# Optimization experiments

Hardware: AMD Instinct MI355X
Metric: run time of the kernel (lower is better)

## Reference

```python
import jax, jax.numpy as jnp
import numpy as np

N_NODES = 50000
N_EDGES = 400000
NUM_FEATURES = 32
NUM_GRAPHS = 64
NUM_CLASSES = 2


def setup_inputs() -> dict:
    key = jax.random.key(0)
    ks = jax.random.split(key, 24)
    inp = {
        "x": jax.random.normal(ks[0], (N_NODES, NUM_FEATURES), dtype=jnp.float32),
        "edge_index": jax.random.randint(ks[1], (2, N_EDGES), 0, N_NODES),
        "edge_attr": jax.random.uniform(ks[2], (N_EDGES, 1), dtype=jnp.float32),
        "batch": jnp.sort(jax.random.randint(ks[3], (N_NODES,), 0, NUM_GRAPHS)),
        # nn1: Linear(1,10) -> ReLU -> Linear(10, 32*16)
        "nn1_w1": jax.random.normal(ks[4], (1, 10), dtype=jnp.float32) * 0.3,
        "nn1_b1": jnp.zeros((10,), jnp.float32),
        "nn1_w2": jax.random.normal(ks[5], (10, NUM_FEATURES * 16), dtype=jnp.float32) * 0.1,
        "nn1_b2": jnp.zeros((NUM_FEATURES * 16,), jnp.float32),
        "conv1_root": jax.random.normal(ks[6], (NUM_FEATURES, 16), dtype=jnp.float32) * 0.1,
        "conv1_bias": jnp.zeros((16,), jnp.float32),
        # nn2: Linear(1,10) -> ReLU -> Linear(10, 16*32)
        "nn2_w1": jax.random.normal(ks[7], (1, 10), dtype=jnp.float32) * 0.3,
        "nn2_b1": jnp.zeros((10,), jnp.float32),
        "nn2_w2": jax.random.normal(ks[8], (10, 16 * 32), dtype=jnp.float32) * 0.1,
        "nn2_b2": jnp.zeros((16 * 32,), jnp.float32),
        "conv2_root": jax.random.normal(ks[9], (16, 32), dtype=jnp.float32) * 0.15,
        "conv2_bias": jnp.zeros((32,), jnp.float32),
        "fc1_w": jax.random.normal(ks[10], (32, 64), dtype=jnp.float32) * 0.15,
        "fc1_b": jnp.zeros((64,), jnp.float32),
        "fc2_w": jax.random.normal(ks[11], (64, NUM_CLASSES), dtype=jnp.float32) * 0.1,
        "fc2_b": jnp.zeros((NUM_CLASSES,), jnp.float32),
    }
    return inp


def _nnconv(x, edge_src, edge_dst, edge_attr, w1, b1, w2, b2, root, bias, in_ch, out_ch):
    # Per-edge weight matrix from edge MLP: [E, in_ch, out_ch]
    h = jax.nn.relu(edge_attr @ w1 + b1) @ w2 + b2
    W = h.reshape(-1, in_ch, out_ch)
    msg = jnp.einsum('ei,eio->eo', x[edge_src], W)  # [E, out_ch]
    agg = jax.ops.segment_sum(msg, edge_dst, num_segments=N_NODES)
    cnt = jax.ops.segment_sum(jnp.ones((msg.shape[0],), x.dtype), edge_dst, num_segments=N_NODES)
    mean = agg / jnp.maximum(cnt, 1.0)[:, None]
    return mean + x @ root + bias


def reference(x, edge_index, edge_attr, batch,
              nn1_w1, nn1_b1, nn1_w2, nn1_b2, conv1_root, conv1_bias,
              nn2_w1, nn2_b1, nn2_w2, nn2_b2, conv2_root, conv2_bias,
              fc1_w, fc1_b, fc2_w, fc2_b):
    src, dst = edge_index[0], edge_index[1]
    h = jax.nn.elu(_nnconv(x, src, dst, edge_attr, nn1_w1, nn1_b1, nn1_w2, nn1_b2,
                           conv1_root, conv1_bias, NUM_FEATURES, 16))
    h = jax.nn.elu(_nnconv(h, src, dst, edge_attr, nn2_w1, nn2_b1, nn2_w2, nn2_b2,
                           conv2_root, conv2_bias, 16, 32))
    # global mean pool over graphs
    gsum = jax.ops.segment_sum(h, batch, num_segments=NUM_GRAPHS)
    gcnt = jax.ops.segment_sum(jnp.ones((h.shape[0],), h.dtype), batch, num_segments=NUM_GRAPHS)
    g = gsum / jnp.maximum(gcnt, 1.0)[:, None]
    g = jax.nn.elu(g @ fc1_w + fc1_b)
    return jax.nn.log_softmax(g @ fc2_w + fc2_b, axis=1)
```

## Files before the change

kernel.cpp:

```cpp
#include <hip/hip_runtime.h>
#include <hip/hip_fp16.h>
#include <math.h>

#define N_NODES 50000
#define N_EDGES 400000
#define NUM_GRAPHS 64
#define NSCAN_BLK ((N_NODES + 1023) / 1024)


__global__ void k_thr(const float* __restrict__ w1a, const float* __restrict__ b1a,
                      const float* __restrict__ w1b, const float* __restrict__ b1b,
                      float* __restrict__ T, int* __restrict__ M) {
    if (threadIdx.x != 0 || blockIdx.x != 0) return;
    for (int layer = 0; layer < 2; layer++) {
        const float* w1 = layer ? w1b : w1a;
        const float* b1 = layer ? b1b : b1a;
        float t[10]; int idx[10];
        for (int j = 0; j < 10; j++) {
            float w = w1[j];
            t[j] = (w != 0.f) ? (-b1[j] / w) : INFINITY;
            idx[j] = j;
        }
        for (int i = 1; i < 10; i++) {
            float tv = t[i]; int iv = idx[i]; int k = i - 1;
            while (k >= 0 && t[k] > tv) { t[k + 1] = t[k]; idx[k + 1] = idx[k]; k--; }
            t[k + 1] = tv; idx[k + 1] = iv;
        }
        int pos[10];
        for (int k = 0; k < 10; k++) pos[idx[k]] = k;
        for (int k = 0; k < 10; k++) T[layer * 10 + k] = t[k];
        for (int kap = 0; kap <= 10; kap++) {
            int m = 0;
            for (int j = 0; j < 10; j++) {
                float w = w1[j];
                bool act = (w > 0.f) ? (pos[j] < kap)
                         : (w < 0.f) ? (pos[j] >= kap)
                         : (b1[j] > 0.f);
                if (act) m |= (1 << j);
            }
            M[layer * 11 + kap] = m;
        }
    }
}

__global__ __launch_bounds__(256) void k0_hist(const int* __restrict__ dst,
        int* __restrict__ cntd) {
    int e = blockIdx.x * 256 + threadIdx.x;
    if (e < N_EDGES) atomicAdd(cntd + dst[e], 1);
}

__global__ __launch_bounds__(1024) void k0_scanA(const int* __restrict__ cntd,
        int* __restrict__ roff, int* __restrict__ woff, int* __restrict__ bsum) {
    __shared__ int tmp[1024];
    int b = blockIdx.x, t = threadIdx.x;
    int n = b * 1024 + t;
    int v = (n < N_NODES) ? cntd[n] : 0;
    tmp[t] = v;
    __syncthreads();
    for (int off = 1; off < 1024; off <<= 1) {
        int add = (t >= off) ? tmp[t - off] : 0;
        __syncthreads();
        tmp[t] += add;
        __syncthreads();
    }
    if (n < N_NODES) { int ex = tmp[t] - v; roff[n] = ex; woff[n] = ex; }
    if (t == 1023) bsum[b] = tmp[1023];
}

__global__ __launch_bounds__(1024) void k0_scanB(const int* __restrict__ bsum,
        int* __restrict__ roff, int* __restrict__ woff) {
    __shared__ int boff;
    int b = blockIdx.x, t = threadIdx.x;
    if (t == 0) {
        int s = 0;
        for (int i = 0; i < b; i++) s += bsum[i];
        boff = s;
    }
    __syncthreads();
    int n = b * 1024 + t;
    if (n < N_NODES) { roff[n] += boff; woff[n] += boff; }
}

__global__ __launch_bounds__(256) void k0_scatter(const int* __restrict__ src,
        const int* __restrict__ dst, const float* __restrict__ ea,
        const float* __restrict__ T, int* __restrict__ woff,
        int* __restrict__ sse1, int* __restrict__ sse2, float* __restrict__ sea) {
    int e = blockIdx.x * 256 + threadIdx.x;
    if (e >= N_EDGES) return;
    int s = src[e], d = dst[e];
    float a = ea[e];
    int k1 = 0, k2 = 0;
#pragma unroll
    for (int j = 0; j < 10; j++) {
        k1 += (T[j] < a);
        k2 += (T[10 + j] < a);
    }
    int pos = atomicAdd(woff + d, 1);
    sse1[pos] = s * 11 + k1;
    sse2[pos] = s * 11 + k2;
    sea[pos] = a;
}

__global__ __launch_bounds__(256) void k1_p1(const float* __restrict__ x,
        const float* __restrict__ w2, const float* __restrict__ b2,
        const float* __restrict__ root, const float* __restrict__ w1,
        const float* __restrict__ b1, const float* __restrict__ bias1,
        const int* __restrict__ M, __half2* __restrict__ tab1,
        float* __restrict__ R1) {
    __shared__ float Wl[32][192];
    __shared__ float xl[16][32];
    __shared__ float w1l[10], b1l[10];
    __shared__ int ml[11];
    int t = threadIdx.x;
    for (int idx = t; idx < 32 * 192; idx += 256) {
        int i = idx / 192, c = idx % 192;
        int m = c >> 4, o = c & 15;
        float w;
        if (m < 10)       w = w2[m * 512 + i * 16 + o];
        else if (m == 10) w = b2[i * 16 + o];
        else              w = root[i * 16 + o];
        Wl[i][c] = w;
    }
    if (t < 10) { w1l[t] = w1[t]; b1l[t] = b1[t]; }
    if (t < 11) ml[t] = M[t];
    int n0 = blockIdx.x * 16;
    for (int idx = t; idx < 16 * 32; idx += 256) {
        int nl = idx >> 5, i = idx & 31;
        int n = n0 + nl;
        xl[nl][i] = (n < N_NODES) ? x[n * 32 + i] : 0.f;
    }
    __syncthreads();
    int nl = t >> 4, o = t & 15;
    int n = n0 + nl;
    if (n >= N_NODES) return;
    float acc[12];
#pragma unroll
    for (int m = 0; m < 12; m++) acc[m] = 0.f;
#pragma unroll
    for (int i = 0; i < 32; i++) {
        float xv = xl[nl][i];
#pragma unroll
        for (int m = 0; m < 12; m++) acc[m] += xv * Wl[i][m * 16 + o];
    }
#pragma unroll
    for (int kap = 0; kap <= 10; kap++) {
        int m = ml[kap];
        float A = 0.f, B = acc[10];
#pragma unroll
        for (int j = 0; j < 10; j++) {
            float f = ((m >> j) & 1) ? 1.f : 0.f;
            A += f * w1l[j] * acc[j];
            B += f * b1l[j] * acc[j];
        }
        tab1[((size_t)(n * 11 + kap)) * 16 + o] = __floats2half2_rn(A, B);
    }
    R1[n * 16 + o] = acc[11] + bias1[o];
}

__global__ __launch_bounds__(256) void k2_edge1(const __half2* __restrict__ tab1,
        const int* __restrict__ roff, const int* __restrict__ sse1,
        const float* __restrict__ sea, const float* __restrict__ R1,
        float* __restrict__ h1) {
    int t = threadIdx.x;
    int d = blockIdx.x * 16 + (t >> 4);
    int o = t & 15;
    if (d >= N_NODES) return;
    int start = roff[d];
    int end = (d == N_NODES - 1) ? N_EDGES : roff[d + 1];
    float acc = 0.f;
    for (int p = start; p < end; ++p) {
        int row = sse1[p];
        float a = sea[p];
        float2 f = __half22float2(tab1[(size_t)row * 16 + o]);
        acc += a * f.x + f.y;
    }
    int deg = end - start;
    float c = (float)(deg > 0 ? deg : 1);
    float v = acc / c + R1[d * 16 + o];
    h1[d * 16 + o] = v > 0.f ? v : expm1f(v);
}

__global__ __launch_bounds__(256) void k4_p2(const float* __restrict__ h1,
        const float* __restrict__ w2, const float* __restrict__ b2,
        const float* __restrict__ root, const float* __restrict__ w1,
        const float* __restrict__ b1, const float* __restrict__ bias2,
        const int* __restrict__ M, __half2* __restrict__ tab2,
        float* __restrict__ R2) {
    __shared__ float Wl[16][384];
    __shared__ float hl[8][16];
    __shared__ float w1l[10], b1l[10];
    __shared__ int ml[11];
    int t = threadIdx.x;
    for (int idx = t; idx < 16 * 384; idx += 256) {
        int i = idx / 384, c = idx % 384;
        int m = c >> 5, o = c & 31;
        float w;
        if (m < 10)       w = w2[m * 512 + i * 32 + o];
        else if (m == 10) w = b2[i * 32 + o];
        else              w = root[i * 32 + o];
        Wl[i][c] = w;
    }
    if (t < 10) { w1l[t] = w1[t]; b1l[t] = b1[t]; }
    if (t < 11) ml[t] = M[11 + t];
    int n0 = blockIdx.x * 8;
    if (t < 128) {
        int nl = t >> 4, i = t & 15;
        int n = n0 + nl;
        hl[nl][i] = (n < N_NODES) ? h1[n * 16 + i] : 0.f;
    }
    __syncthreads();
    int nl = t >> 5, o = t & 31;
    int n = n0 + nl;
    if (n >= N_NODES) return;
    float acc[12];
#pragma unroll
    for (int m = 0; m < 12; m++) acc[m] = 0.f;
#pragma unroll
    for (int i = 0; i < 16; i++) {
        float hv = hl[nl][i];
#pragma unroll
        for (int m = 0; m < 12; m++) acc[m] += hv * Wl[i][m * 32 + o];
    }
#pragma unroll
    for (int kap = 0; kap <= 10; kap++) {
        int m = ml[kap];
        float A = 0.f, B = acc[10];
#pragma unroll
        for (int j = 0; j < 10; j++) {
            float f = ((m >> j) & 1) ? 1.f : 0.f;
            A += f * w1l[j] * acc[j];
            B += f * b1l[j] * acc[j];
        }
        tab2[((size_t)(n * 11 + kap)) * 32 + o] = __floats2half2_rn(A, B);
    }
    R2[(size_t)n * 32 + o] = acc[11] + bias2[o];
}

__global__ __launch_bounds__(256) void k5_edge2(const __half2* __restrict__ tab2,
        const int* __restrict__ roff, const int* __restrict__ sse2,
        const float* __restrict__ sea, const float* __restrict__ R2,
        float* __restrict__ h2) {
    int t = threadIdx.x;
    int d = blockIdx.x * 8 + (t >> 5);
    int o = t & 31;
    if (d >= N_NODES) return;
    int start = roff[d];
    int end = (d == N_NODES - 1) ? N_EDGES : roff[d + 1];
    float acc = 0.f;
    for (int p = start; p < end; ++p) {
        int row = sse2[p];
        float a = sea[p];
        float2 f = __half22float2(tab2[(size_t)row * 32 + o]);
        acc += a * f.x + f.y;
    }
    int deg = end - start;
    float c = (float)(deg > 0 ? deg : 1);
    float v = acc / c + R2[(size_t)d * 32 + o];
    h2[(size_t)d * 32 + o] = v > 0.f ? v : expm1f(v);
}

__global__ __launch_bounds__(256) void k6_partial(const float* __restrict__ h2,
        const int* __restrict__ batch, float* __restrict__ gsum) {
    const int NB = 512;
    const int chunk = (N_NODES + NB - 1) / NB;
    int begin = blockIdx.x * chunk;
    int end = begin + chunk;
    if (end > N_NODES) end = N_NODES;
    int t = threadIdx.x;
    int o = t & 31, ch = t >> 5;
    float acc = 0.f;
    int cur_g = -1;
    for (int n = begin + ch; n < end; n += 8) {
        int g = batch[n];
        float v = h2[(size_t)n * 32 + o];
        if (g != cur_g) {
            if (cur_g >= 0) atomicAdd(gsum + cur_g * 32 + o, acc);
            cur_g = g; acc = 0.f;
        }
        acc += v;
    }
    if (cur_g >= 0) atomicAdd(gsum + cur_g * 32 + o, acc);
}

__global__ __launch_bounds__(256) void k8_head(const float* __restrict__ gsum,
        const int* __restrict__ batch,
        const float* __restrict__ fc1w, const float* __restrict__ fc1b,
        const float* __restrict__ fc2w, const float* __restrict__ fc2b,
        float* __restrict__ out) {
    __shared__ float gl[64][32];
    __shared__ float w1l[32][64];
    __shared__ float hl[64][64];
    __shared__ float zl[64][2];
    __shared__ float gc[64];
    int t = threadIdx.x;
    if (t < 64) {
        int g = t;
        int lo = 0, hi = N_NODES;
        while (lo < hi) { int mid = (lo + hi) >> 1; if (batch[mid] < g) lo = mid + 1; else hi = mid; }
        int s0 = lo;
        lo = 0; hi = N_NODES;
        while (lo < hi) { int mid = (lo + hi) >> 1; if (batch[mid] < g + 1) lo = mid + 1; else hi = mid; }
        gc[g] = fmaxf((float)(lo - s0), 1.0f);
    }
    for (int idx = t; idx < 32 * 64; idx += 256) w1l[idx >> 6][idx & 63] = fc1w[idx];
    __syncthreads();
    for (int idx = t; idx < 64 * 32; idx += 256) gl[idx >> 5][idx & 31] = gsum[idx] / gc[idx >> 5];
    __syncthreads();
    for (int idx = t; idx < 64 * 64; idx += 256) {
        int gg = idx >> 6, c = idx & 63;
        float acc = fc1b[c];
#pragma unroll
        for (int i = 0; i < 32; i++) acc += gl[gg][i] * w1l[i][c];
        hl[gg][c] = acc > 0.f ? acc : expm1f(acc);
    }
    __syncthreads();
    if (t < 128) {
        int gg = t >> 1, k = t & 1;
        float acc = fc2b[k];
#pragma unroll
        for (int c = 0; c < 64; c++) acc += hl[gg][c] * fc2w[c * 2 + k];
        zl[gg][k] = acc;
    }
    __syncthreads();
    if (t < 128) {
        int gg = t >> 1, k = t & 1;
        float z0 = zl[gg][0], z1 = zl[gg][1];
        float m = fmaxf(z0, z1);
        float lse = m + logf(expf(z0 - m) + expf(z1 - m));
        out[t] = zl[gg][k] - lse;
    }
}

extern "C" void kernel_launch(void* const* d_in, const int* in_sizes, int n_in,
                              void* d_out, int out_size, void* d_ws, size_t ws_size,
                              hipStream_t stream) {
    const float* x       = (const float*)d_in[0];
    const int*   ei      = (const int*)d_in[1];
    const float* ea      = (const float*)d_in[2];
    const int*   batch   = (const int*)d_in[3];
    const float* nn1_w1  = (const float*)d_in[4];
    const float* nn1_b1  = (const float*)d_in[5];
    const float* nn1_w2  = (const float*)d_in[6];
    const float* nn1_b2  = (const float*)d_in[7];
    const float* c1_root = (const float*)d_in[8];
    const float* c1_bias = (const float*)d_in[9];
    const float* nn2_w1  = (const float*)d_in[10];
    const float* nn2_b1  = (const float*)d_in[11];
    const float* nn2_w2  = (const float*)d_in[12];
    const float* nn2_b2  = (const float*)d_in[13];
    const float* c2_root = (const float*)d_in[14];
    const float* c2_bias = (const float*)d_in[15];
    const float* fc1w    = (const float*)d_in[16];
    const float* fc1b    = (const float*)d_in[17];
    const float* fc2w    = (const float*)d_in[18];
    const float* fc2b    = (const float*)d_in[19];
    const int* src = ei;
    const int* dst = ei + N_EDGES;

    char* ws = (char*)d_ws;
    size_t off = 0;
    __half2* tab1 = (__half2*)(ws + off); off += (size_t)N_NODES * 11 * 16 * 4;
    __half2* tab2 = (__half2*)(ws + off); off += (size_t)N_NODES * 11 * 32 * 4;
    float* R1   = (float*)(ws + off); off += (size_t)N_NODES * 16 * 4;
    float* R2   = (float*)(ws + off); off += (size_t)N_NODES * 32 * 4;
    float* h1   = (float*)(ws + off); off += (size_t)N_NODES * 16 * 4;
    float* h2   = (float*)(ws + off); off += (size_t)N_NODES * 32 * 4;
    int*   roff = (int*)(ws + off);   off += (size_t)N_NODES * 4;
    int*   woff = (int*)(ws + off);   off += (size_t)N_NODES * 4;
    int*   bsum = (int*)(ws + off);   off += (size_t)NSCAN_BLK * 4;
    int*   sse1 = (int*)(ws + off);   off += (size_t)N_EDGES * 4;
    int*   sse2 = (int*)(ws + off);   off += (size_t)N_EDGES * 4;
    float* sea  = (float*)(ws + off); off += (size_t)N_EDGES * 4;
    float* thrT = (float*)(ws + off); off += 20 * 4;
    int*   thrM = (int*)(ws + off);   off += 22 * 4;
    off = (off + 255) & ~(size_t)255;
    char* zbase = ws + off;
    int*   cntd = (int*)(ws + off);   off += (size_t)N_NODES * 4;
    float* gsum = (float*)(ws + off); off += (size_t)NUM_GRAPHS * 32 * 4;
    size_t zbytes = (size_t)(ws + off - zbase);

    hipMemsetAsync(zbase, 0, zbytes, stream);

    k_thr<<<1, 64, 0, stream>>>(nn1_w1, nn1_b1, nn2_w1, nn2_b1, thrT, thrM);
    k0_hist<<<(N_EDGES + 255) / 256, 256, 0, stream>>>(dst, cntd);
    k0_scanA<<<NSCAN_BLK, 1024, 0, stream>>>(cntd, roff, woff, bsum);
    k0_scanB<<<NSCAN_BLK, 1024, 0, stream>>>(bsum, roff, woff);
    k0_scatter<<<(N_EDGES + 255) / 256, 256, 0, stream>>>(src, dst, ea, thrT, woff, sse1, sse2, sea);
    k1_p1<<<(N_NODES + 15) / 16, 256, 0, stream>>>(x, nn1_w2, nn1_b2, c1_root,
            nn1_w1, nn1_b1, c1_bias, thrM, tab1, R1);
    k2_edge1<<<(N_NODES + 15) / 16, 256, 0, stream>>>(tab1, roff, sse1, sea, R1, h1);
    k4_p2<<<(N_NODES + 7) / 8, 256, 0, stream>>>(h1, nn2_w2, nn2_b2, c2_root,
            nn2_w1, nn2_b1, c2_bias, thrM, tab2, R2);
    k5_edge2<<<(N_NODES + 7) / 8, 256, 0, stream>>>(tab2, roff, sse2, sea, R2, h2);
    k6_partial<<<512, 256, 0, stream>>>(h2, batch, gsum);
    k8_head<<<1, 256, 0, stream>>>(gsum, batch, fc1w, fc1b, fc2w, fc2b, (float*)d_out);
}
```

Measured before the change: 334.9 us.

## Skip unused ReLU-pattern table slices and switch table layout to slice-major

The edge scatter now records, through a block-shared OR and one global atomic per block, which ReLU activation patterns (threshold intervals) any edge actually hits. The per-node precompute kernels then write only the table slices for patterns in use, and the layout changes from node-major to pattern-major (kap*N_NODES+n). The aim is to cut table writes and memory footprint when edge attributes span few intervals. The cost is extra shared and global atomics in the scatter plus a divergent branch per slice. The pattern-major layout also changes how gathers in the edge kernels hit cache.

```diff
diff --git a/kernel.cpp b/kernel.cpp
--- a/kernel.cpp
+++ b/kernel.cpp
@@ -84,29 +84,39 @@
 __global__ __launch_bounds__(256) void k0_scatter(const int* __restrict__ src,
         const int* __restrict__ dst, const float* __restrict__ ea,
         const float* __restrict__ T, int* __restrict__ woff,
-        int* __restrict__ sse1, int* __restrict__ sse2, float* __restrict__ sea) {
-    int e = blockIdx.x * 256 + threadIdx.x;
-    if (e >= N_EDGES) return;
-    int s = src[e], d = dst[e];
-    float a = ea[e];
-    int k1 = 0, k2 = 0;
-#pragma unroll
-    for (int j = 0; j < 10; j++) {
-        k1 += (T[j] < a);
-        k2 += (T[10 + j] < a);
-    }
-    int pos = atomicAdd(woff + d, 1);
-    sse1[pos] = s * 11 + k1;
-    sse2[pos] = s * 11 + k2;
-    sea[pos] = a;
+        int* __restrict__ sse1, int* __restrict__ sse2, float* __restrict__ sea,
+        int* __restrict__ U) {
+    __shared__ int um0, um1;
+    int t = threadIdx.x;
+    if (t == 0) { um0 = 0; um1 = 0; }
+    __syncthreads();
+    int e = blockIdx.x * 256 + t;
+    if (e < N_EDGES) {
+        int s = src[e], d = dst[e];
+        float a = ea[e];
+        int k1 = 0, k2 = 0;
+#pragma unroll
+        for (int j = 0; j < 10; j++) {
+            k1 += (T[j] < a);
+            k2 += (T[10 + j] < a);
+        }
+        int pos = atomicAdd(woff + d, 1);
+        sse1[pos] = k1 * N_NODES + s;
+        sse2[pos] = k2 * N_NODES + s;
+        sea[pos] = a;
+        atomicOr(&um0, 1 << k1);
+        atomicOr(&um1, 1 << k2);
+    }
+    __syncthreads();
+    if (t == 0) { atomicOr(U + 0, um0); atomicOr(U + 1, um1); }
 }
 
 __global__ __launch_bounds__(256) void k1_p1(const float* __restrict__ x,
         const float* __restrict__ w2, const float* __restrict__ b2,
         const float* __restrict__ root, const float* __restrict__ w1,
         const float* __restrict__ b1, const float* __restrict__ bias1,
-        const int* __restrict__ M, __half2* __restrict__ tab1,
-        float* __restrict__ R1) {
+        const int* __restrict__ M, const int* __restrict__ U,
+        __half2* __restrict__ tab1, float* __restrict__ R1) {
     __shared__ float Wl[32][192];
     __shared__ float xl[16][32];
     __shared__ float w1l[10], b1l[10];
@@ -130,6 +140,7 @@
         xl[nl][i] = (n < N_NODES) ? x[n * 32 + i] : 0.f;
     }
     __syncthreads();
+    int used = U[0];
     int nl = t >> 4, o = t & 15;
     int n = n0 + nl;
     if (n >= N_NODES) return;
@@ -142,17 +153,20 @@
 #pragma unroll
         for (int m = 0; m < 12; m++) acc[m] += xv * Wl[i][m * 16 + o];
     }
+    float wj[10], bj[10];
+#pragma unroll
+    for (int j = 0; j < 10; j++) { wj[j] = w1l[j] * acc[j]; bj[j] = b1l[j] * acc[j]; }
 #pragma unroll
     for (int kap = 0; kap <= 10; kap++) {
-        int m = ml[kap];
-        float A = 0.f, B = acc[10];
-#pragma unroll
-        for (int j = 0; j < 10; j++) {
-            float f = ((m >> j) & 1) ? 1.f : 0.f;
-            A += f * w1l[j] * acc[j];
-            B += f * b1l[j] * acc[j];
-        }
-        tab1[((size_t)(n * 11 + kap)) * 16 + o] = __floats2half2_rn(A, B);
+        if ((used >> kap) & 1) {
+            int m = ml[kap];
+            float A = 0.f, B = acc[10];
+#pragma unroll
+            for (int j = 0; j < 10; j++) {
+                if ((m >> j) & 1) { A += wj[j]; B += bj[j]; }
+            }
+            tab1[((size_t)kap * N_NODES + n) * 16 + o] = __floats2half2_rn(A, B);
+        }
     }
     R1[n * 16 + o] = acc[11] + bias1[o];
 }
@@ -184,8 +198,8 @@
         const float* __restrict__ w2, const float* __restrict__ b2,
         const float* __restrict__ root, const float* __restrict__ w1,
         const float* __restrict__ b1, const float* __restrict__ bias2,
-        const int* __restrict__ M, __half2* __restrict__ tab2,
-        float* __restrict__ R2) {
+        const int* __restrict__ M, const int* __restrict__ U,
+        __half2* __restrict__ tab2, float* __restrict__ R2) {
     __shared__ float Wl[16][384];
     __shared__ float hl[8][16];
     __shared__ float w1l[10], b1l[10];
@@ -209,6 +223,7 @@
         hl[nl][i] = (n < N_NODES) ? h1[n * 16 + i] : 0.f;
     }
     __syncthreads();
+    int used = U[1];
     int nl = t >> 5, o = t & 31;
     int n = n0 + nl;
     if (n >= N_NODES) return;
@@ -221,17 +236,20 @@
 #pragma unroll
         for (int m = 0; m < 12; m++) acc[m] += hv * Wl[i][m * 32 + o];
     }
+    float wj[10], bj[10];
+#pragma unroll
+    for (int j = 0; j < 10; j++) { wj[j] = w1l[j] * acc[j]; bj[j] = b1l[j] * acc[j]; }
 #pragma unroll
     for (int kap = 0; kap <= 10; kap++) {
-        int m = ml[kap];
-        float A = 0.f, B = acc[10];
-#pragma unroll
-        for (int j = 0; j < 10; j++) {
-            float f = ((m >> j) & 1) ? 1.f : 0.f;
-            A += f * w1l[j] * acc[j];
-            B += f * b1l[j] * acc[j];
-        }
-        tab2[((size_t)(n * 11 + kap)) * 32 + o] = __floats2half2_rn(A, B);
+        if ((used >> kap) & 1) {
+            int m = ml[kap];
+            float A = 0.f, B = acc[10];
+#pragma unroll
+            for (int j = 0; j < 10; j++) {
+                if ((m >> j) & 1) { A += wj[j]; B += bj[j]; }
+            }
+            tab2[((size_t)kap * N_NODES + n) * 32 + o] = __floats2half2_rn(A, B);
+        }
     }
     R2[(size_t)n * 32 + o] = acc[11] + bias2[o];
 }
@@ -377,6 +395,7 @@
     char* zbase = ws + off;
     int*   cntd = (int*)(ws + off);   off += (size_t)N_NODES * 4;
     float* gsum = (float*)(ws + off); off += (size_t)NUM_GRAPHS * 32 * 4;
+    int*   thrU = (int*)(ws + off);   off += 2 * 4;
     size_t zbytes = (size_t)(ws + off - zbase);
 
     hipMemsetAsync(zbase, 0, zbytes, stream);
@@ -385,12 +404,13 @@
     k0_hist<<<(N_EDGES + 255) / 256, 256, 0, stream>>>(dst, cntd);
     k0_scanA<<<NSCAN_BLK, 1024, 0, stream>>>(cntd, roff, woff, bsum);
     k0_scanB<<<NSCAN_BLK, 1024, 0, stream>>>(bsum, roff, woff);
-    k0_scatter<<<(N_EDGES + 255) / 256, 256, 0, stream>>>(src, dst, ea, thrT, woff, sse1, sse2, sea);
+    k0_scatter<<<(N_EDGES + 255) / 256, 256, 0, stream>>>(src, dst, ea, thrT, woff,
+            sse1, sse2, sea, thrU);
     k1_p1<<<(N_NODES + 15) / 16, 256, 0, stream>>>(x, nn1_w2, nn1_b2, c1_root,
-            nn1_w1, nn1_b1, c1_bias, thrM, tab1, R1);
+            nn1_w1, nn1_b1, c1_bias, thrM, thrU, tab1, R1);
     k2_edge1<<<(N_NODES + 15) / 16, 256, 0, stream>>>(tab1, roff, sse1, sea, R1, h1);
     k4_p2<<<(N_NODES + 7) / 8, 256, 0, stream>>>(h1, nn2_w2, nn2_b2, c2_root,
-            nn2_w1, nn2_b1, c2_bias, thrM, tab2, R2);
+            nn2_w1, nn2_b1, c2_bias, thrM, thrU, tab2, R2);
     k5_edge2<<<(N_NODES + 7) / 8, 256, 0, stream>>>(tab2, roff, sse2, sea, R2, h2);
     k6_partial<<<512, 256, 0, stream>>>(h2, batch, gsum);
     k8_head<<<1, 256, 0, stream>>>(gsum, batch, fc1w, fc1b, fc2w, fc2b, (float*)d_out);
```

Measured after the change: 332.3 us. No clear change (-0.8%).
